# Performance work log

Measured on AMD Instinct MI355X. Metric: run time of the kernel, lower is better.

Reference implementation:

```python
import jax, jax.numpy as jnp
import numpy as np

N_VERTS = 40962  # icosphere level-6 vertex count
K_RING = 19      # 2-ring filter size


def setup_inputs() -> dict:
    key = jax.random.key(0)
    k1, k2, k3, k4 = jax.random.split(key, 4)
    B, C_in, C_out = 4, 64, 64
    x = jax.random.normal(k1, (B, C_in, N_VERTS), dtype=jnp.float32)
    neigh_orders = jax.random.randint(k2, (N_VERTS, K_RING), 0, N_VERTS, dtype=jnp.int32)
    # nn.Linear(19*in_feats, out_feats): weight [C_out, 19*C_in], bias [C_out]
    fan_in = K_RING * C_in
    bound = 1.0 / np.sqrt(fan_in)
    W = jax.random.uniform(k3, (C_out, fan_in), dtype=jnp.float32, minval=-bound, maxval=bound)
    b = jax.random.uniform(k4, (C_out,), dtype=jnp.float32, minval=-bound, maxval=bound)
    return {"x": x, "neigh_orders": neigh_orders, "W": W, "b": b}


def reference(x, neigh_orders, W, b):
    # x: [B, C_in, N] -> [B, N, C_in]
    xt = jnp.transpose(x, (0, 2, 1))
    B, N, C = xt.shape
    # gather 19-ring neighbors: [B, N, 19, C_in]
    gathered = xt[:, neigh_orders, :]
    # im2col-style flatten: [B, N, 19*C_in]
    mat = gathered.reshape(B, N, K_RING * C)
    # Linear: mat @ W.T + b -> [B, N, C_out]
    out = jnp.einsum('bnk,ok->bno', mat, W) + b
    # back to [B, C_out, N]
    return jnp.transpose(out, (0, 2, 1))
```

## Files before the change

kernel.cpp:

```cpp
#include <hip/hip_runtime.h>
#include <hip/hip_bf16.h>


#define NV   40962
#define KR   19
#define CIN  64
#define COUT 64
#define NB   4
#define NTILES 321

typedef __bf16 bf16;
typedef __bf16 bf16x8 __attribute__((ext_vector_type(8)));
typedef float  floatx4 __attribute__((ext_vector_type(4)));

#define XT_ELEMS ((size_t)NB * NV * CIN)
#define WB_OFF   ((XT_ELEMS * 2 + 255) & ~(size_t)255)
#define WS_NEED  (WB_OFF + (size_t)COUT * KR * CIN * 2)

__global__ __launch_bounds__(256) void transpose_kernel(
    const float* __restrict__ x, bf16* __restrict__ xt)
{
    __shared__ float tile[64 * 65];
    const int b  = blockIdx.y;
    const int v0 = blockIdx.x * 64;
    const int t  = threadIdx.x;

    const int vl = t & 63;
    const int c0 = t >> 6;
    const int vg = min(v0 + vl, NV - 1);
    #pragma unroll
    for (int p = 0; p < 16; ++p) {
        int c = c0 * 16 + p;
        tile[vl * 65 + c] = x[((size_t)(b * CIN + c)) * NV + vg];
    }
    __syncthreads();

    const int v = t >> 2;
    const int q = t & 3;
    if (v0 + v < NV) {
        #pragma unroll
        for (int p = 0; p < 2; ++p) {
            int chunk = q + p * 4;
            bf16x8 o;
            #pragma unroll
            for (int j = 0; j < 8; ++j)
                o[j] = (bf16)tile[v * 65 + chunk * 8 + j];
            *(bf16x8*)&xt[((size_t)(b * NV + v0 + v)) * 64 + chunk * 8] = o;
        }
    }
}

__global__ __launch_bounds__(256) void convw_kernel(
    const float* __restrict__ W, bf16* __restrict__ Wb)
{
    int i = blockIdx.x * 256 + threadIdx.x;
    const int total4 = COUT * KR * CIN / 4;
    if (i < total4) {
        float4 v = ((const float4*)W)[i];
        bf16* p = Wb + (size_t)i * 4;
        p[0] = (bf16)v.x; p[1] = (bf16)v.y; p[2] = (bf16)v.z; p[3] = (bf16)v.w;
    }
}

__global__ __launch_bounds__(256, 4) void conv_kernel(
    const int*   __restrict__ neigh,
    const bf16*  __restrict__ xt,
    const bf16*  __restrict__ Wb,
    const float* __restrict__ bias,
    float*       __restrict__ out)
{
    __shared__ alignas(16) bf16 Wlds[2][2][4096];

    const int i    = blockIdx.x;
    const int b    = (i & 7) >> 1;
    const int tile = (i >> 3) * 2 + (i & 1);
    if (tile >= NTILES) return;
    const int n0   = tile * 128;

    const int t    = threadIdx.x;
    const int wv   = t >> 6;
    const int lane = t & 63;
    const int l15  = lane & 15;
    const int g    = lane >> 4;

    int nn[2], ib[2];
    #pragma unroll
    for (int s = 0; s < 2; ++s) {
        nn[s] = n0 + wv * 32 + s * 16 + l15;
        ib[s] = min(nn[s], NV - 1) * KR;
    }

    const bf16* xb = xt + (((size_t)b * NV) << 6) + g * 8;

    const int srow = t >> 2;
    const int c4   = t & 3;
    const int skc  = c4 >> 1;
    const int sg0  = (c4 & 1) * 2;
    const int sot  = srow >> 4, sl15 = srow & 15;
    const int sdst0 = ((sot * 2 + skc) * 64 + (sg0 + 0) * 16 + sl15) * 8;
    const int sdst1 = ((sot * 2 + skc) * 64 + (sg0 + 1) * 16 + sl15) * 8;
    const bf16* sw = Wb + (size_t)srow * (KR * 64) + c4 * 16;

    floatx4 acc[2][4];
    #pragma unroll
    for (int s = 0; s < 2; ++s)
        #pragma unroll
        for (int o = 0; o < 4; ++o)
            acc[s][o] = (floatx4){0.f, 0.f, 0.f, 0.f};

    bf16x8 xf[2][2][2];
    bf16x8 xg[2][2][2];

    #pragma unroll
    for (int j = 0; j < 2; ++j) {
        bf16x8 w0 = *(const bf16x8*)(sw + j * 64);
        bf16x8 w1 = *(const bf16x8*)(sw + j * 64 + 8);
        *(bf16x8*)(&Wlds[0][j][sdst0]) = w0;
        *(bf16x8*)(&Wlds[0][j][sdst1]) = w1;
        #pragma unroll
        for (int s = 0; s < 2; ++s) {
            int v = neigh[ib[s] + j];
            v = ((unsigned)v < (unsigned)NV) ? v : 0;
            const bf16* p = xb + ((size_t)v << 6);
            xf[j][s][0] = *(const bf16x8*)(p);
            xf[j][s][1] = *(const bf16x8*)(p + 32);
        }
    }
    __syncthreads();

    #pragma unroll
    for (int rp = 0; rp < 10; ++rp) {
        const int st = rp & 1;

        if (rp + 1 < 10) {
            #pragma unroll
            for (int j = 0; j < 2; ++j) {
                const int ring = 2 * (rp + 1) + j;
                if (ring < KR) {
                    bf16x8 w0 = *(const bf16x8*)(sw + ring * 64);
                    bf16x8 w1 = *(const bf16x8*)(sw + ring * 64 + 8);
                    *(bf16x8*)(&Wlds[st ^ 1][j][sdst0]) = w0;
                    *(bf16x8*)(&Wlds[st ^ 1][j][sdst1]) = w1;
                    #pragma unroll
                    for (int s = 0; s < 2; ++s) {
                        int v = neigh[ib[s] + ring];
                        v = ((unsigned)v < (unsigned)NV) ? v : 0;
                        const bf16* p = xb + ((size_t)v << 6);
                        xg[j][s][0] = *(const bf16x8*)(p);
                        xg[j][s][1] = *(const bf16x8*)(p + 32);
                    }
                }
            }
        }

        #pragma unroll
        for (int j = 0; j < 2; ++j) {
            const int ring = 2 * rp + j;
            if (ring < KR) {
                const bf16* wbase = &Wlds[st][j][lane * 8];
                #pragma unroll
                for (int ot = 0; ot < 4; ++ot) {
                    #pragma unroll
                    for (int kc = 0; kc < 2; ++kc) {
                        bf16x8 wf = *(const bf16x8*)(wbase + (ot * 2 + kc) * 512);
                        #pragma unroll
                        for (int s = 0; s < 2; ++s) {
                            acc[s][ot] = __builtin_amdgcn_mfma_f32_16x16x32_bf16(
                                wf, xf[j][s][kc], acc[s][ot], 0, 0, 0);
                        }
                    }
                }
            }
        }
        __syncthreads();

        #pragma unroll
        for (int j = 0; j < 2; ++j)
            #pragma unroll
            for (int s = 0; s < 2; ++s) {
                xf[j][s][0] = xg[j][s][0];
                xf[j][s][1] = xg[j][s][1];
            }
    }

    #pragma unroll
    for (int ot = 0; ot < 4; ++ot) {
        #pragma unroll
        for (int ii = 0; ii < 4; ++ii) {
            int o = ot * 16 + g * 4 + ii;
            float bv = bias[o];
            #pragma unroll
            for (int s = 0; s < 2; ++s) {
                if (nn[s] < NV) {
                    out[((size_t)(b * COUT + o)) * NV + nn[s]] =
                        acc[s][ot][ii] + bv;
                }
            }
        }
    }
}

__global__ __launch_bounds__(64) void fallback_kernel(
    const int*   __restrict__ neigh,
    const float* __restrict__ x,
    const float* __restrict__ W,
    const float* __restrict__ bias,
    float*       __restrict__ out)
{
    __shared__ float xg[KR * CIN];
    const int bn = blockIdx.x;
    const int b  = bn / NV;
    const int n  = bn % NV;
    const int t  = threadIdx.x;

    for (int k = t; k < KR * CIN; k += 64) {
        int r = k / CIN, c = k - r * CIN;
        int v = neigh[n * KR + r];
        v = ((unsigned)v < (unsigned)NV) ? v : 0;
        xg[k] = x[((size_t)(b * CIN + c)) * NV + v];
    }
    __syncthreads();

    float s = bias[t];
    const float* wrow = W + (size_t)t * (KR * CIN);
    for (int k = 0; k < KR * CIN; ++k) s += xg[k] * wrow[k];
    out[((size_t)(b * COUT + t)) * NV + n] = s;
}

extern "C" void kernel_launch(void* const* d_in, const int* in_sizes, int n_in,
                              void* d_out, int out_size, void* d_ws, size_t ws_size,
                              hipStream_t stream)
{
    const float* x     = (const float*)d_in[0];
    const int*   neigh = (const int*)d_in[1];
    const float* W     = (const float*)d_in[2];
    const float* bias  = (const float*)d_in[3];
    float* out = (float*)d_out;

    if (d_ws != nullptr && ws_size >= WS_NEED) {
        bf16* xt = (bf16*)d_ws;
        bf16* Wb = (bf16*)((char*)d_ws + WB_OFF);

        dim3 tgrid((NV + 63) / 64, NB);
        transpose_kernel<<<tgrid, 256, 0, stream>>>(x, xt);
        convw_kernel<<<(COUT * KR * CIN / 4 + 255) / 256, 256, 0, stream>>>(W, Wb);

        int nblk = 8 * ((NTILES + 1) / 2);
        conv_kernel<<<nblk, 256, 0, stream>>>(neigh, xt, Wb, bias, out);
    } else {
        fallback_kernel<<<NB * NV, 64, 0, stream>>>(neigh, x, W, bias, out);
    }
}
```

Measured before the change: 169.0 us.

## Pre-swizzle weights into MFMA fragment layout and load directly, drop LDS staging

The weight conversion kernel now writes bf16 weights already arranged in per-lane MFMA fragment order, so the conv kernel can load weight fragments straight from global memory (L2-resident) into registers instead of staging them through double-buffered LDS with barriers. Each wave now handles 64 vertices instead of 32, doubling the accumulators and reusing each weight fragment across four vertex subtiles. The ring loop is per-ring with register prefetch of the next ring's gathers and weights. This removes LDS traffic and __syncthreads but raises register pressure (occupancy hint lowered to 2) and repeats global weight loads in every wave.

```diff
diff --git a/kernel.cpp b/kernel.cpp
--- a/kernel.cpp
+++ b/kernel.cpp
@@ -7,7 +7,7 @@
 #define CIN  64
 #define COUT 64
 #define NB   4
-#define NTILES 321
+#define NT256 161
 
 typedef __bf16 bf16;
 typedef __bf16 bf16x8 __attribute__((ext_vector_type(8)));
@@ -51,31 +51,37 @@
 }
 
 __global__ __launch_bounds__(256) void convw_kernel(
-    const float* __restrict__ W, bf16* __restrict__ Wb)
-{
-    int i = blockIdx.x * 256 + threadIdx.x;
-    const int total4 = COUT * KR * CIN / 4;
-    if (i < total4) {
-        float4 v = ((const float4*)W)[i];
-        bf16* p = Wb + (size_t)i * 4;
-        p[0] = (bf16)v.x; p[1] = (bf16)v.y; p[2] = (bf16)v.z; p[3] = (bf16)v.w;
-    }
-}
-
-__global__ __launch_bounds__(256, 4) void conv_kernel(
+    const float* __restrict__ W, bf16* __restrict__ Wf)
+{
+    const int idx = blockIdx.x * 256 + threadIdx.x;
+    if (idx >= KR * 8 * 64) return;
+    const int lane = idx & 63;
+    const int f    = (idx >> 6) & 7;
+    const int ring = idx >> 9;
+    const int ot   = f >> 1;
+    const int kc   = f & 1;
+    const int row  = ot * 16 + (lane & 15);
+    const int col0 = ring * 64 + kc * 32 + (lane >> 4) * 8;
+    const float* src = W + (size_t)row * (KR * CIN) + col0;
+    float4 a = *(const float4*)(src);
+    float4 c = *(const float4*)(src + 4);
+    bf16x8 o;
+    o[0] = (bf16)a.x; o[1] = (bf16)a.y; o[2] = (bf16)a.z; o[3] = (bf16)a.w;
+    o[4] = (bf16)c.x; o[5] = (bf16)c.y; o[6] = (bf16)c.z; o[7] = (bf16)c.w;
+    *(bf16x8*)(Wf + (size_t)idx * 8) = o;
+}
+
+__global__ __launch_bounds__(256, 2) void conv_kernel(
     const int*   __restrict__ neigh,
     const bf16*  __restrict__ xt,
-    const bf16*  __restrict__ Wb,
+    const bf16*  __restrict__ Wf,
     const float* __restrict__ bias,
     float*       __restrict__ out)
 {
-    __shared__ alignas(16) bf16 Wlds[2][2][4096];
-
     const int i    = blockIdx.x;
     const int b    = (i & 7) >> 1;
     const int tile = (i >> 3) * 2 + (i & 1);
-    if (tile >= NTILES) return;
-    const int n0   = tile * 128;
+    if (tile >= NT256) return;
 
     const int t    = threadIdx.x;
     const int wv   = t >> 6;
@@ -83,114 +89,87 @@
     const int l15  = lane & 15;
     const int g    = lane >> 4;
 
-    int nn[2], ib[2];
-    #pragma unroll
-    for (int s = 0; s < 2; ++s) {
-        nn[s] = n0 + wv * 32 + s * 16 + l15;
+    const int n0 = tile * 256 + wv * 64;
+
+    int nn[4], ib[4];
+    #pragma unroll
+    for (int s = 0; s < 4; ++s) {
+        nn[s] = n0 + s * 16 + l15;
         ib[s] = min(nn[s], NV - 1) * KR;
     }
 
     const bf16* xb = xt + (((size_t)b * NV) << 6) + g * 8;
-
-    const int srow = t >> 2;
-    const int c4   = t & 3;
-    const int skc  = c4 >> 1;
-    const int sg0  = (c4 & 1) * 2;
-    const int sot  = srow >> 4, sl15 = srow & 15;
-    const int sdst0 = ((sot * 2 + skc) * 64 + (sg0 + 0) * 16 + sl15) * 8;
-    const int sdst1 = ((sot * 2 + skc) * 64 + (sg0 + 1) * 16 + sl15) * 8;
-    const bf16* sw = Wb + (size_t)srow * (KR * 64) + c4 * 16;
-
-    floatx4 acc[2][4];
-    #pragma unroll
-    for (int s = 0; s < 2; ++s)
+    const bf16* wb = Wf + lane * 8;
+
+    floatx4 acc[4][4];
+    #pragma unroll
+    for (int s = 0; s < 4; ++s)
         #pragma unroll
         for (int o = 0; o < 4; ++o)
             acc[s][o] = (floatx4){0.f, 0.f, 0.f, 0.f};
 
-    bf16x8 xf[2][2][2];
-    bf16x8 xg[2][2][2];
-
-    #pragma unroll
-    for (int j = 0; j < 2; ++j) {
-        bf16x8 w0 = *(const bf16x8*)(sw + j * 64);
-        bf16x8 w1 = *(const bf16x8*)(sw + j * 64 + 8);
-        *(bf16x8*)(&Wlds[0][j][sdst0]) = w0;
-        *(bf16x8*)(&Wlds[0][j][sdst1]) = w1;
-        #pragma unroll
-        for (int s = 0; s < 2; ++s) {
-            int v = neigh[ib[s] + j];
-            v = ((unsigned)v < (unsigned)NV) ? v : 0;
-            const bf16* p = xb + ((size_t)v << 6);
-            xf[j][s][0] = *(const bf16x8*)(p);
-            xf[j][s][1] = *(const bf16x8*)(p + 32);
-        }
-    }
-    __syncthreads();
-
-    #pragma unroll
-    for (int rp = 0; rp < 10; ++rp) {
-        const int st = rp & 1;
-
-        if (rp + 1 < 10) {
-            #pragma unroll
-            for (int j = 0; j < 2; ++j) {
-                const int ring = 2 * (rp + 1) + j;
-                if (ring < KR) {
-                    bf16x8 w0 = *(const bf16x8*)(sw + ring * 64);
-                    bf16x8 w1 = *(const bf16x8*)(sw + ring * 64 + 8);
-                    *(bf16x8*)(&Wlds[st ^ 1][j][sdst0]) = w0;
-                    *(bf16x8*)(&Wlds[st ^ 1][j][sdst1]) = w1;
-                    #pragma unroll
-                    for (int s = 0; s < 2; ++s) {
-                        int v = neigh[ib[s] + ring];
-                        v = ((unsigned)v < (unsigned)NV) ? v : 0;
-                        const bf16* p = xb + ((size_t)v << 6);
-                        xg[j][s][0] = *(const bf16x8*)(p);
-                        xg[j][s][1] = *(const bf16x8*)(p + 32);
-                    }
-                }
+    bf16x8 xf[4][2];
+    bf16x8 wf[8];
+
+    #pragma unroll
+    for (int s = 0; s < 4; ++s) {
+        int v = neigh[ib[s]];
+        v = ((unsigned)v < (unsigned)NV) ? v : 0;
+        const bf16* p = xb + ((size_t)v << 6);
+        xf[s][0] = *(const bf16x8*)(p);
+        xf[s][1] = *(const bf16x8*)(p + 32);
+    }
+    #pragma unroll
+    for (int f = 0; f < 8; ++f)
+        wf[f] = *(const bf16x8*)(wb + f * 512);
+
+    #pragma unroll
+    for (int r = 0; r < KR; ++r) {
+        bf16x8 xg[4][2], wg[8];
+        if (r + 1 < KR) {
+            #pragma unroll
+            for (int s = 0; s < 4; ++s) {
+                int v = neigh[ib[s] + r + 1];
+                v = ((unsigned)v < (unsigned)NV) ? v : 0;
+                const bf16* p = xb + ((size_t)v << 6);
+                xg[s][0] = *(const bf16x8*)(p);
+                xg[s][1] = *(const bf16x8*)(p + 32);
             }
-        }
-
-        #pragma unroll
-        for (int j = 0; j < 2; ++j) {
-            const int ring = 2 * rp + j;
-            if (ring < KR) {
-                const bf16* wbase = &Wlds[st][j][lane * 8];
+            const bf16* wr = wb + (size_t)(r + 1) * (8 * 512);
+            #pragma unroll
+            for (int f = 0; f < 8; ++f)
+                wg[f] = *(const bf16x8*)(wr + f * 512);
+        }
+
+        #pragma unroll
+        for (int kc = 0; kc < 2; ++kc)
+            #pragma unroll
+            for (int ot = 0; ot < 4; ++ot)
                 #pragma unroll
-                for (int ot = 0; ot < 4; ++ot) {
-                    #pragma unroll
-                    for (int kc = 0; kc < 2; ++kc) {
-                        bf16x8 wf = *(const bf16x8*)(wbase + (ot * 2 + kc) * 512);
-                        #pragma unroll
-                        for (int s = 0; s < 2; ++s) {
-                            acc[s][ot] = __builtin_amdgcn_mfma_f32_16x16x32_bf16(
-                                wf, xf[j][s][kc], acc[s][ot], 0, 0, 0);
-                        }
-                    }
-                }
+                for (int s = 0; s < 4; ++s)
+                    acc[s][ot] = __builtin_amdgcn_mfma_f32_16x16x32_bf16(
+                        wf[ot * 2 + kc], xf[s][kc], acc[s][ot], 0, 0, 0);
+
+        if (r + 1 < KR) {
+            #pragma unroll
+            for (int s = 0; s < 4; ++s) {
+                xf[s][0] = xg[s][0];
+                xf[s][1] = xg[s][1];
             }
-        }
-        __syncthreads();
-
-        #pragma unroll
-        for (int j = 0; j < 2; ++j)
-            #pragma unroll
-            for (int s = 0; s < 2; ++s) {
-                xf[j][s][0] = xg[j][s][0];
-                xf[j][s][1] = xg[j][s][1];
-            }
+            #pragma unroll
+            for (int f = 0; f < 8; ++f)
+                wf[f] = wg[f];
+        }
     }
 
     #pragma unroll
     for (int ot = 0; ot < 4; ++ot) {
         #pragma unroll
         for (int ii = 0; ii < 4; ++ii) {
-            int o = ot * 16 + g * 4 + ii;
-            float bv = bias[o];
-            #pragma unroll
-            for (int s = 0; s < 2; ++s) {
+            const int o = ot * 16 + g * 4 + ii;
+            const float bv = bias[o];
+            #pragma unroll
+            for (int s = 0; s < 4; ++s) {
                 if (nn[s] < NV) {
                     out[((size_t)(b * COUT + o)) * NV + nn[s]] =
                         acc[s][ot][ii] + bv;
@@ -239,14 +218,14 @@
 
     if (d_ws != nullptr && ws_size >= WS_NEED) {
         bf16* xt = (bf16*)d_ws;
-        bf16* Wb = (bf16*)((char*)d_ws + WB_OFF);
+        bf16* Wf = (bf16*)((char*)d_ws + WB_OFF);
 
         dim3 tgrid((NV + 63) / 64, NB);
         transpose_kernel<<<tgrid, 256, 0, stream>>>(x, xt);
-        convw_kernel<<<(COUT * KR * CIN / 4 + 255) / 256, 256, 0, stream>>>(W, Wb);
-
-        int nblk = 8 * ((NTILES + 1) / 2);
-        conv_kernel<<<nblk, 256, 0, stream>>>(neigh, xt, Wb, bias, out);
+        convw_kernel<<<(KR * 8 * 64 + 255) / 256, 256, 0, stream>>>(W, Wf);
+
+        int nblk = 8 * ((NT256 + 1) / 2);
+        conv_kernel<<<nblk, 256, 0, stream>>>(neigh, xt, Wf, bias, out);
     } else {
         fallback_kernel<<<NB * NV, 64, 0, stream>>>(neigh, x, W, bias, out);
     }
```

Result: slower. 185.2 us (+9.6%).
